# Kernel tuning notes

Hardware: AMD Instinct MI355X
Metric: run time of the kernel (lower is better)

The kernel has to match this reference:

```python
import jax, jax.numpy as jnp
import numpy as np


def _linear_init(key, fan_in, fan_out):
    k1, k2 = jax.random.split(key)
    sc = 1.0 / np.sqrt(fan_in)
    w = jax.random.uniform(k1, (fan_in, fan_out), jnp.float32, -sc, sc)
    b = jax.random.uniform(k2, (fan_out,), jnp.float32, -sc, sc)
    return w, b


def setup_inputs() -> dict:
    key = jax.random.key(0)
    ks = jax.random.split(key, 16)
    b, s, q, c, d = 8, 5, 15, 256, 4
    inp = {
        'support_xf': jax.random.normal(ks[0], (b, s, c, d, d), jnp.float32),
        'query_xf': jax.random.normal(ks[1], (b, q, c, d, d), jnp.float32),
        'support_y': jax.random.randint(ks[2], (b, s), 0, 5),
        'query_y': jax.random.randint(ks[3], (b, q), 0, 5),
    }
    g_dims = [(516, 256), (256, 256), (256, 256), (256, 256)]
    for i, (fi, fo) in enumerate(g_dims):
        w, bb = _linear_init(ks[4 + i], fi, fo)
        inp['g_w%d' % (i + 1)] = w
        inp['g_b%d' % (i + 1)] = bb
    f_dims = [(256, 256), (256, 256), (256, 29), (29, 1)]
    for i, (fi, fo) in enumerate(f_dims):
        w, bb = _linear_init(ks[8 + i], fi, fo)
        inp['f_w%d' % (i + 1)] = w
        inp['f_b%d' % (i + 1)] = bb
    return inp


def reference(support_xf, query_xf, support_y, query_y,
              g_w1, g_b1, g_w2, g_b2, g_w3, g_b3, g_w4, g_b4,
              f_w1, f_b1, f_w2, f_b2, f_w3, f_b3, f_w4, f_b4):
    b, s, c, d, _ = support_xf.shape
    q = query_xf.shape[1]
    d2 = d * d
    relu = jax.nn.relu
    # coord channels: ch0 = i/d (row), ch1 = j/d (col), shape [2, d, d]
    ii = jnp.arange(d, dtype=support_xf.dtype) / d
    coord = jnp.stack([jnp.broadcast_to(ii[:, None], (d, d)),
                       jnp.broadcast_to(ii[None, :], (d, d))], axis=0)
    sup = jnp.concatenate([support_xf, jnp.broadcast_to(coord, (b, s, 2, d, d))], axis=2)
    qry = jnp.concatenate([query_xf, jnp.broadcast_to(coord, (b, q, 2, d, d))], axis=2)
    cp = c + 2
    sup = sup.reshape(b, s, cp, d2).transpose(0, 1, 3, 2)  # [b,s,d2,cp]
    qry = qry.reshape(b, q, cp, d2).transpose(0, 1, 3, 2)  # [b,q,d2,cp]
    # pair[b,q,s,m,n] = concat(support feature at spatial n, query feature at spatial m)
    sup_e = jnp.broadcast_to(sup[:, None, :, None, :, :], (b, q, s, d2, d2, cp))
    qry_e = jnp.broadcast_to(qry[:, :, None, :, None, :], (b, q, s, d2, d2, cp))
    x = jnp.concatenate([sup_e, qry_e], axis=-1)  # [b,q,s,d2,d2,2*cp]
    # g MLP applied per pair
    x = relu(x @ g_w1 + g_b1)
    x = relu(x @ g_w2 + g_b2)
    x = relu(x @ g_w3 + g_b3)
    x = relu(x @ g_w4 + g_b4)
    xf = x.sum(axis=(3, 4))  # sum over d^4 pairs -> [b,q,s,256]
    # f MLP (Dropout is identity in eval mode)
    y = relu(xf @ f_w1 + f_b1)
    y = relu(y @ f_w2 + f_b2)
    y = relu(y @ f_w3 + f_b3)
    score = jax.nn.sigmoid(y @ f_w4 + f_b4)[..., 0]  # [b,q,s]
    label = (support_y[:, None, :] == query_y[:, :, None]).astype(score.dtype)
    loss = jnp.sum((label - score) ** 2) / b
    return loss
```

## Files before the change

### kernel.cpp

```cpp
#include <hip/hip_runtime.h>

typedef __attribute__((ext_vector_type(8))) __bf16 bf16x8;
typedef __attribute__((ext_vector_type(8))) short short8;
typedef __attribute__((ext_vector_type(4))) float f32x4;
typedef unsigned int u32;

static __device__ __forceinline__ unsigned short f2bf(float f) {
    u32 u = __float_as_uint(f);
    u += 0x7FFFu + ((u >> 16) & 1u);
    return (unsigned short)(u >> 16);
}
static __device__ __forceinline__ u32 cvt_pk_bf16(float lo, float hi) {
    u32 r;
    asm("v_cvt_pk_bf16_f32 %0, %1, %2" : "=v"(r) : "v"(lo), "v"(hi));
    return r;
}
static __device__ __forceinline__ bf16x8 as_bf16x8(short8 v) {
    return __builtin_bit_cast(bf16x8, v);
}
static __device__ __forceinline__ f32x4 mfma16(short8 a, short8 b, f32x4 c) {
    return __builtin_amdgcn_mfma_f32_16x16x32_bf16(as_bf16x8(a), as_bf16x8(b), c, 0, 0, 0);
}

#define NB 8
#define NS 5
#define NQ 15
#define A_OFF_F 0
#define B_OFF_F (640*256)
#define XF_OFF_F (B_OFF_F + 1920*256)
#define WF_OFF_BYTES ((XF_OFF_F + 600*1024)*4)
#define WF1_OFF_BYTES (WF_OFF_BYTES + 48*8192)
#define WFF_OFF_BYTES (WF1_OFF_BYTES + 32*9216)
#define WF3_OFF_BYTES (WFF_OFF_BYTES + 32*8192)

__global__ void kA(const float* __restrict__ w2, const float* __restrict__ w3,
                   const float* __restrict__ w4, const float* __restrict__ w1,
                   const float* __restrict__ fw1, const float* __restrict__ fw2,
                   const float* __restrict__ fw3,
                   unsigned short* __restrict__ wf, unsigned short* __restrict__ wf1,
                   unsigned short* __restrict__ wff, unsigned short* __restrict__ wf3) {
    int bid = blockIdx.x;
    int l = threadIdx.x;
    if (bid < 48) {
        int L = bid >> 4, tt = bid & 15;
        const float* W = (L == 0) ? w2 : ((L == 1) ? w3 : w4);
        int nn = tt * 16 + (l & 15);
        #pragma unroll
        for (int kk = 0; kk < 8; ++kk) {
            int k0 = kk * 32 + (l >> 4) * 8;
            short8 ov;
            #pragma unroll
            for (int j = 0; j < 8; ++j)
                ov[j] = (short)f2bf(W[(size_t)(k0 + j) * 256 + nn]);
            *(short8*)((char*)wf + (size_t)bid * 8192 + kk * 1024 + l * 16) = ov;
        }
        return;
    }
    if (bid < 80) {
        int c1 = bid - 48;
        int S = c1 >> 4, tt = c1 & 15;
        int nn = tt * 16 + (l & 15);
        for (int kk = 0; kk < 9; ++kk) {
            int k0 = kk * 32 + (l >> 4) * 8;
            short8 ov;
            #pragma unroll
            for (int j = 0; j < 8; ++j) {
                int kb = k0 + j;
                float v = (kb < 258) ? w1[(size_t)(S * 258 + kb) * 256 + nn] : 0.0f;
                ov[j] = (short)f2bf(v);
            }
            *(short8*)((char*)wf1 + (size_t)c1 * 9216 + kk * 1024 + l * 16) = ov;
        }
        return;
    }
    if (bid < 112) {
        int cid = bid - 80;
        int Lf = cid >> 4, tt = cid & 15;
        const float* W = (Lf == 0) ? fw1 : fw2;
        int nn = tt * 16 + (l & 15);
        #pragma unroll
        for (int kk = 0; kk < 8; ++kk) {
            int k0 = kk * 32 + (l >> 4) * 8;
            short8 ov;
            #pragma unroll
            for (int j = 0; j < 8; ++j)
                ov[j] = (short)f2bf(W[(size_t)(k0 + j) * 256 + nn]);
            *(short8*)((char*)wff + (size_t)cid * 8192 + kk * 1024 + l * 16) = ov;
        }
        return;
    }
    {
        int tt = bid - 112;
        int nn = tt * 16 + (l & 15);
        #pragma unroll
        for (int kk = 0; kk < 8; ++kk) {
            int k0 = kk * 32 + (l >> 4) * 8;
            short8 ov;
            #pragma unroll
            for (int j = 0; j < 8; ++j) {
                float v = (nn < 29) ? fw3[(size_t)(k0 + j) * 29 + nn] : 0.0f;
                ov[j] = (short)f2bf(v);
            }
            *(short8*)((char*)wf3 + (size_t)tt * 8192 + kk * 1024 + l * 16) = ov;
        }
    }
}

__launch_bounds__(512, 1)
__global__ void kB(const float* __restrict__ sup, const float* __restrict__ qry,
                   const unsigned short* __restrict__ wf1,
                   const float* __restrict__ gb1, float* __restrict__ ws) {
    __shared__ short Xf[18432];
    int bid = blockIdx.x;
    bool isA = (bid < 10);
    int S = isA ? 0 : 1;
    int cellbase = isA ? bid * 4 : (bid - 10) * 4;
    const float* src = isA ? sup : qry;
    float* dst0 = ws + (isA ? A_OFF_F : B_OFF_F);
    int t = threadIdx.x;
    int w = t >> 6, l = t & 63;
    int g = l >> 4, c = l & 15;
    char* Xb = (char*)Xf;
    const char* w1b = (const char*)wf1;

    for (int idx = w; idx < 36; idx += 8) {
        int m = idx / 9, kk = idx % 9;
        const float* xp = src + (size_t)(cellbase + m) * 4096;
        int kbase = kk * 32 + g * 8;
        float v[8];
        #pragma unroll
        for (int j = 0; j < 8; ++j) {
            int kb = kbase + j;
            float x;
            if (kb < 256)       x = xp[(size_t)kb * 16 + c];
            else if (kb == 256) x = (float)(c >> 2) * 0.25f;
            else if (kb == 257) x = (float)(c & 3) * 0.25f;
            else                x = 0.0f;
            v[j] = x;
        }
        uint4 hv;
        hv.x = cvt_pk_bf16(v[0], v[1]);
        hv.y = cvt_pk_bf16(v[2], v[3]);
        hv.z = cvt_pk_bf16(v[4], v[5]);
        hv.w = cvt_pk_bf16(v[6], v[7]);
        *(uint4*)(Xb + (size_t)(m * 9 + kk) * 1024 + l * 16) = hv;
    }
    __syncthreads();

    int wp = w >> 2, wn = w & 3;
    const char* wbase = w1b + (size_t)(S * 16 + wn * 4) * 9216;
    short8 wcur[4];
    #pragma unroll
    for (int tti = 0; tti < 4; ++tti)
        wcur[tti] = *(const short8*)(wbase + (size_t)tti * 9216 + l * 16);

    f32x4 acc[2][4];
    #pragma unroll
    for (int pg = 0; pg < 2; ++pg)
        #pragma unroll
        for (int tti = 0; tti < 4; ++tti)
            acc[pg][tti] = (f32x4){0.f, 0.f, 0.f, 0.f};

    #pragma unroll
    for (int kk = 0; kk < 9; ++kk) {
        int kn = kk + 1; if (kn > 8) kn = 8;
        short8 wnxt[4];
        #pragma unroll
        for (int tti = 0; tti < 4; ++tti)
            wnxt[tti] = *(const short8*)(wbase + (size_t)tti * 9216 + kn * 1024 + l * 16);
        #pragma unroll
        for (int pg = 0; pg < 2; ++pg) {
            short8 h = *(const short8*)(Xb + (size_t)((wp * 2 + pg) * 9 + kk) * 1024 + l * 16);
            #pragma unroll
            for (int tti = 0; tti < 4; ++tti)
                acc[pg][tti] = mfma16(wcur[tti], h, acc[pg][tti]);
        }
        #pragma unroll
        for (int tti = 0; tti < 4; ++tti) wcur[tti] = wnxt[tti];
    }

    #pragma unroll
    for (int tti = 0; tti < 4; ++tti) {
        int col0 = wn * 64 + tti * 16 + g * 4;
        float4 bv = {0.f, 0.f, 0.f, 0.f};
        if (S == 0) bv = *(const float4*)(gb1 + col0);
        #pragma unroll
        for (int pg = 0; pg < 2; ++pg) {
            int row = (cellbase + wp * 2 + pg) * 16 + c;
            float4 o;
            o.x = acc[pg][tti][0] + bv.x;
            o.y = acc[pg][tti][1] + bv.y;
            o.z = acc[pg][tti][2] + bv.z;
            o.w = acc[pg][tti][3] + bv.w;
            *(float4*)(dst0 + (size_t)row * 256 + col0) = o;
        }
    }
}

__launch_bounds__(512, 4)
__global__ void k3_g(const float* __restrict__ wsA, const float* __restrict__ wsB,
                     const unsigned short* __restrict__ wf,
                     const float* __restrict__ gb2, const float* __restrict__ gb3,
                     const float* __restrict__ gb4, float* __restrict__ xf) {
    __shared__ short Hf[32768];
    __shared__ float bs[768];
    int bid = blockIdx.x;
    int bqs = bid >> 1, half = bid & 1;
    int b = bqs / 75, rem = bqs % 75, qi = rem / 5, si = rem % 5;
    int t = threadIdx.x;
    int w = t >> 6, l = t & 63;
    int g = l >> 4, c = l & 15;
    int wp = w >> 2, wn = w & 3;
    char* Hb = (char*)Hf;
    const char* wfb = (const char*)wf;

    if (t < 256) { bs[t] = gb2[t]; bs[256 + t] = gb3[t]; bs[512 + t] = gb4[t]; }

    short8 wcur[4];
    #pragma unroll
    for (int tti = 0; tti < 4; ++tti)
        wcur[tti] = *(const short8*)(wfb + (size_t)(wn * 4 + tti) * 8192 + l * 16);

    {
        const float* Arow = wsA + (size_t)(b * NS + si) * 4096 + c * 256;
        const float* Brow = wsB + (size_t)(b * NQ + qi) * 4096 + (half * 8 + w) * 256;
        #pragma unroll
        for (int kk = 0; kk < 8; ++kk) {
            const float* ap = Arow + kk * 32 + g * 8;
            const float* bp = Brow + kk * 32 + g * 8;
            float4 a0 = *(const float4*)ap, a1 = *(const float4*)(ap + 4);
            float4 b0 = *(const float4*)bp, b1 = *(const float4*)(bp + 4);
            uint4 hv;
            hv.x = cvt_pk_bf16(fmaxf(a0.x + b0.x, 0.f), fmaxf(a0.y + b0.y, 0.f));
            hv.y = cvt_pk_bf16(fmaxf(a0.z + b0.z, 0.f), fmaxf(a0.w + b0.w, 0.f));
            hv.z = cvt_pk_bf16(fmaxf(a1.x + b1.x, 0.f), fmaxf(a1.y + b1.y, 0.f));
            hv.w = cvt_pk_bf16(fmaxf(a1.z + b1.z, 0.f), fmaxf(a1.w + b1.w, 0.f));
            *(uint4*)(Hb + (size_t)(w * 8 + kk) * 1024 + l * 16) = hv;
        }
    }
    __syncthreads();

    #pragma unroll 1
    for (int L = 0; L < 3; ++L) {
        f32x4 acc[4][4];
        #pragma unroll
        for (int pg = 0; pg < 4; ++pg)
            #pragma unroll
            for (int tti = 0; tti < 4; ++tti)
                acc[pg][tti] = (f32x4){0.f, 0.f, 0.f, 0.f};

        #pragma unroll
        for (int kk = 0; kk < 8; ++kk) {
            int s = L * 8 + kk + 1; if (s > 23) s = 23;
            int Ln = s >> 3, kn = s & 7;
            short8 wnxt[4];
            #pragma unroll
            for (int tti = 0; tti < 4; ++tti)
                wnxt[tti] = *(const short8*)(wfb +
                    (size_t)(Ln * 16 + wn * 4 + tti) * 8192 + kn * 1024 + l * 16);
            #pragma unroll
            for (int pg = 0; pg < 4; ++pg) {
                short8 h = *(const short8*)(Hb +
                    (size_t)((wp * 4 + pg) * 8 + kk) * 1024 + l * 16);
                #pragma unroll
                for (int tti = 0; tti < 4; ++tti)
                    acc[pg][tti] = mfma16(wcur[tti], h, acc[pg][tti]);
            }
            #pragma unroll
            for (int tti = 0; tti < 4; ++tti) wcur[tti] = wnxt[tti];
        }

        float4 bv[4];
        #pragma unroll
        for (int tti = 0; tti < 4; ++tti)
            bv[tti] = *(const float4*)(bs + L * 256 + wn * 64 + tti * 16 + g * 4);

        if (L < 2) {
            __syncthreads();
            #pragma unroll
            for (int pg = 0; pg < 4; ++pg) {
                int m = wp * 4 + pg;
                #pragma unroll
                for (int tti = 0; tti < 4; ++tti) {
                    uint2 q;
                    q.x = cvt_pk_bf16(fmaxf(acc[pg][tti][0] + bv[tti].x, 0.f),
                                      fmaxf(acc[pg][tti][1] + bv[tti].y, 0.f));
                    q.y = cvt_pk_bf16(fmaxf(acc[pg][tti][2] + bv[tti].z, 0.f),
                                      fmaxf(acc[pg][tti][3] + bv[tti].w, 0.f));
                    int kk2 = wn * 2 + (tti >> 1);
                    int dlane = ((tti & 1) * 2 + (g >> 1)) * 16 + c;
                    *(uint2*)(Hb + (size_t)(m * 8 + kk2) * 1024 + dlane * 16 + (g & 1) * 8) = q;
                }
            }
            __syncthreads();
        } else {
            #pragma unroll
            for (int tti = 0; tti < 4; ++tti) {
                float s0 = 0.f, s1 = 0.f, s2 = 0.f, s3 = 0.f;
                #pragma unroll
                for (int pg = 0; pg < 4; ++pg) {
                    s0 += fmaxf(acc[pg][tti][0] + bv[tti].x, 0.f);
                    s1 += fmaxf(acc[pg][tti][1] + bv[tti].y, 0.f);
                    s2 += fmaxf(acc[pg][tti][2] + bv[tti].z, 0.f);
                    s3 += fmaxf(acc[pg][tti][3] + bv[tti].w, 0.f);
                }
                #pragma unroll
                for (int d = 1; d < 16; d <<= 1) {
                    s0 += __shfl_xor(s0, d); s1 += __shfl_xor(s1, d);
                    s2 += __shfl_xor(s2, d); s3 += __shfl_xor(s3, d);
                }
                if (c == 0) {
                    float4 o = {s0, s1, s2, s3};
                    *(float4*)(xf + (((size_t)bqs * 2 + half) * 2 + wp) * 256 +
                               wn * 64 + tti * 16 + g * 4) = o;
                }
            }
        }
    }
}

__launch_bounds__(512, 1)
__global__ void k4_f(const float* __restrict__ xf,
                     const unsigned short* __restrict__ wff,
                     const unsigned short* __restrict__ wf3,
                     const float* __restrict__ fb1, const float* __restrict__ fb2,
                     const float* __restrict__ fb3,
                     const float* __restrict__ fw4, const float* __restrict__ fb4,
                     const int* __restrict__ sy, const int* __restrict__ qy,
                     float* __restrict__ out) {
    __shared__ short Hf[16384];
    __shared__ float bs[512];
    __shared__ float bs3[32];
    __shared__ float y3[64][32];
    int bid = blockIdx.x;
    int t = threadIdx.x;
    int w = t >> 6, l = t & 63;
    int g = l >> 4, c = l & 15;
    char* Hb = (char*)Hf;
    const char* wfb = (const char*)wff;

    bs[t & 511] = (t < 256) ? fb1[t] : fb2[t - 256];
    if (t < 32) bs3[t] = (t < 29) ? fb3[t] : 0.0f;

    for (int fi = w; fi < 32; fi += 8) {
        int m = fi >> 3, kk = fi & 7;
        int row = bid * 64 + m * 16 + c;
        if (row > 599) row = 599;
        const float* xr = xf + (size_t)row * 1024;
        int kb = kk * 32 + g * 8;
        float v[8];
        #pragma unroll
        for (int j = 0; j < 8; ++j) {
            int f = kb + j;
            v[j] = xr[f] + xr[256 + f] + xr[512 + f] + xr[768 + f];
        }
        uint4 hv;
        hv.x = cvt_pk_bf16(v[0], v[1]);
        hv.y = cvt_pk_bf16(v[2], v[3]);
        hv.z = cvt_pk_bf16(v[4], v[5]);
        hv.w = cvt_pk_bf16(v[6], v[7]);
        *(uint4*)(Hb + (size_t)(m * 8 + kk) * 1024 + l * 16) = hv;
    }
    __syncthreads();

    int wp = w >> 2, wn = w & 3;
    short8 wcur[4];
    #pragma unroll
    for (int tti = 0; tti < 4; ++tti)
        wcur[tti] = *(const short8*)(wfb + (size_t)(wn * 4 + tti) * 8192 + l * 16);

    #pragma unroll 1
    for (int L = 0; L < 2; ++L) {
        f32x4 acc[2][4];
        #pragma unroll
        for (int pg = 0; pg < 2; ++pg)
            #pragma unroll
            for (int tti = 0; tti < 4; ++tti)
                acc[pg][tti] = (f32x4){0.f, 0.f, 0.f, 0.f};

        #pragma unroll
        for (int kk = 0; kk < 8; ++kk) {
            int s = L * 8 + kk + 1; if (s > 15) s = 15;
            int Ln = s >> 3, kn = s & 7;
            short8 wnxt[4];
            #pragma unroll
            for (int tti = 0; tti < 4; ++tti)
                wnxt[tti] = *(const short8*)(wfb +
                    (size_t)(Ln * 16 + wn * 4 + tti) * 8192 + kn * 1024 + l * 16);
            #pragma unroll
            for (int pg = 0; pg < 2; ++pg) {
                short8 h = *(const short8*)(Hb +
                    (size_t)((wp * 2 + pg) * 8 + kk) * 1024 + l * 16);
                #pragma unroll
                for (int tti = 0; tti < 4; ++tti)
                    acc[pg][tti] = mfma16(wcur[tti], h, acc[pg][tti]);
            }
            #pragma unroll
            for (int tti = 0; tti < 4; ++tti) wcur[tti] = wnxt[tti];
        }

        float4 bv[4];
        #pragma unroll
        for (int tti = 0; tti < 4; ++tti)
            bv[tti] = *(const float4*)(bs + L * 256 + wn * 64 + tti * 16 + g * 4);

        __syncthreads();
        #pragma unroll
        for (int pg = 0; pg < 2; ++pg) {
            int m = wp * 2 + pg;
            #pragma unroll
            for (int tti = 0; tti < 4; ++tti) {
                uint2 q;
                q.x = cvt_pk_bf16(fmaxf(acc[pg][tti][0] + bv[tti].x, 0.f),
                                  fmaxf(acc[pg][tti][1] + bv[tti].y, 0.f));
                q.y = cvt_pk_bf16(fmaxf(acc[pg][tti][2] + bv[tti].z, 0.f),
                                  fmaxf(acc[pg][tti][3] + bv[tti].w, 0.f));
                int kk2 = wn * 2 + (tti >> 1);
                int dlane = ((tti & 1) * 2 + (g >> 1)) * 16 + c;
                *(uint2*)(Hb + (size_t)(m * 8 + kk2) * 1024 + dlane * 16 + (g & 1) * 8) = q;
            }
        }
        __syncthreads();
    }

    {
        int m = w >> 1, tt = w & 1;
        f32x4 a3 = {0.f, 0.f, 0.f, 0.f};
        #pragma unroll
        for (int kk = 0; kk < 8; ++kk) {
            short8 wv = *(const short8*)((const char*)wf3 +
                (size_t)(tt * 8 + kk) * 1024 + l * 16);
            short8 h = *(const short8*)(Hb + (size_t)(m * 8 + kk) * 1024 + l * 16);
            a3 = mfma16(wv, h, a3);
        }
        #pragma unroll
        for (int r = 0; r < 4; ++r) {
            int oc = tt * 16 + g * 4 + r;
            float v = a3[r] + bs3[oc];
            y3[m * 16 + c][oc] = v > 0.f ? v : 0.f;
        }
    }
    __syncthreads();

    if (t < 64) {
        int bqs = bid * 64 + t;
        if (bqs < 600) {
            float z = fb4[0];
            #pragma unroll
            for (int k = 0; k < 29; ++k) z += y3[t][k] * fw4[k];
            float score = 1.0f / (1.0f + __expf(-z));
            int b = bqs / 75, rem = bqs % 75, qi = rem / 5, si = rem % 5;
            float label = (sy[b * NS + si] == qy[b * NQ + qi]) ? 1.0f : 0.0f;
            float d = label - score;
            atomicAdd(out, d * d * 0.125f);
        }
    }
}

extern "C" void kernel_launch(void* const* d_in, const int* in_sizes, int n_in,
                              void* d_out, int out_size, void* d_ws, size_t ws_size,
                              hipStream_t stream) {
    const float* sup = (const float*)d_in[0];
    const float* qry = (const float*)d_in[1];
    const int*   sy  = (const int*)d_in[2];
    const int*   qy  = (const int*)d_in[3];
    const float* gw1 = (const float*)d_in[4];
    const float* gb1 = (const float*)d_in[5];
    const float* gw2 = (const float*)d_in[6];
    const float* gb2 = (const float*)d_in[7];
    const float* gw3 = (const float*)d_in[8];
    const float* gb3 = (const float*)d_in[9];
    const float* gw4 = (const float*)d_in[10];
    const float* gb4 = (const float*)d_in[11];
    const float* fw1 = (const float*)d_in[12];
    const float* fb1 = (const float*)d_in[13];
    const float* fw2 = (const float*)d_in[14];
    const float* fb2 = (const float*)d_in[15];
    const float* fw3 = (const float*)d_in[16];
    const float* fb3 = (const float*)d_in[17];
    const float* fw4 = (const float*)d_in[18];
    const float* fb4 = (const float*)d_in[19];

    float* ws = (float*)d_ws;
    float* A  = ws + A_OFF_F;
    float* B  = ws + B_OFF_F;
    float* xf = ws + XF_OFF_F;
    unsigned short* wf  = (unsigned short*)((char*)d_ws + WF_OFF_BYTES);
    unsigned short* wf1 = (unsigned short*)((char*)d_ws + WF1_OFF_BYTES);
    unsigned short* wff = (unsigned short*)((char*)d_ws + WFF_OFF_BYTES);
    unsigned short* wf3 = (unsigned short*)((char*)d_ws + WF3_OFF_BYTES);
    float* out = (float*)d_out;

    hipMemsetAsync(out, 0, sizeof(float), stream);

    kA<<<114, 64, 0, stream>>>(gw2, gw3, gw4, gw1, fw1, fw2, fw3, wf, wf1, wff, wf3);
    kB<<<40, 512, 0, stream>>>(sup, qry, wf1, gb1, ws);
    k3_g<<<1200, 512, 0, stream>>>(A, B, wf, gb2, gb3, gb4, xf);
    k4_f<<<10, 512, 0, stream>>>(xf, wff, wf3, fb1, fb2, fb3, fw4, fb4, sy, qy, out);
}
```

Baseline: 118.9 us.

## Split prep kernels: spread layer-1 GEMM over more blocks, fold weight packing and memset

```diff
diff --git a/kernel.cpp b/kernel.cpp
--- a/kernel.cpp
+++ b/kernel.cpp
@@ -33,106 +33,105 @@
 #define WFF_OFF_BYTES (WF1_OFF_BYTES + 32*9216)
 #define WF3_OFF_BYTES (WFF_OFF_BYTES + 32*8192)
 
-__global__ void kA(const float* __restrict__ w2, const float* __restrict__ w3,
-                   const float* __restrict__ w4, const float* __restrict__ w1,
+__global__ void kA(const float* __restrict__ w1, unsigned short* __restrict__ wf1) {
+    int c1 = blockIdx.x;
+    int l = threadIdx.x;
+    int S = c1 >> 4, tt = c1 & 15;
+    int nn = tt * 16 + (l & 15);
+    for (int kk = 0; kk < 9; ++kk) {
+        int k0 = kk * 32 + (l >> 4) * 8;
+        short8 ov;
+        #pragma unroll
+        for (int j = 0; j < 8; ++j) {
+            int kb = k0 + j;
+            float v = (kb < 258) ? w1[(size_t)(S * 258 + kb) * 256 + nn] : 0.0f;
+            ov[j] = (short)f2bf(v);
+        }
+        *(short8*)((char*)wf1 + (size_t)c1 * 9216 + kk * 1024 + l * 16) = ov;
+    }
+}
+
+__global__ void kB(const float* __restrict__ sup, const float* __restrict__ qry,
+                   const unsigned short* __restrict__ wf1, const float* __restrict__ gb1,
+                   const float* __restrict__ w2, const float* __restrict__ w3,
+                   const float* __restrict__ w4,
                    const float* __restrict__ fw1, const float* __restrict__ fw2,
                    const float* __restrict__ fw3,
-                   unsigned short* __restrict__ wf, unsigned short* __restrict__ wf1,
-                   unsigned short* __restrict__ wff, unsigned short* __restrict__ wf3) {
+                   float* __restrict__ ws, unsigned short* __restrict__ wf,
+                   unsigned short* __restrict__ wff, unsigned short* __restrict__ wf3,
+                   float* __restrict__ out) {
+    __shared__ short Xf[4608];
     int bid = blockIdx.x;
-    int l = threadIdx.x;
-    if (bid < 48) {
-        int L = bid >> 4, tt = bid & 15;
-        const float* W = (L == 0) ? w2 : ((L == 1) ? w3 : w4);
-        int nn = tt * 16 + (l & 15);
-        #pragma unroll
-        for (int kk = 0; kk < 8; ++kk) {
-            int k0 = kk * 32 + (l >> 4) * 8;
-            short8 ov;
-            #pragma unroll
-            for (int j = 0; j < 8; ++j)
-                ov[j] = (short)f2bf(W[(size_t)(k0 + j) * 256 + nn]);
-            *(short8*)((char*)wf + (size_t)bid * 8192 + kk * 1024 + l * 16) = ov;
-        }
-        return;
-    }
-    if (bid < 80) {
-        int c1 = bid - 48;
-        int S = c1 >> 4, tt = c1 & 15;
-        int nn = tt * 16 + (l & 15);
-        for (int kk = 0; kk < 9; ++kk) {
-            int k0 = kk * 32 + (l >> 4) * 8;
-            short8 ov;
-            #pragma unroll
-            for (int j = 0; j < 8; ++j) {
-                int kb = k0 + j;
-                float v = (kb < 258) ? w1[(size_t)(S * 258 + kb) * 256 + nn] : 0.0f;
-                ov[j] = (short)f2bf(v);
-            }
-            *(short8*)((char*)wf1 + (size_t)c1 * 9216 + kk * 1024 + l * 16) = ov;
-        }
-        return;
-    }
-    if (bid < 112) {
-        int cid = bid - 80;
-        int Lf = cid >> 4, tt = cid & 15;
-        const float* W = (Lf == 0) ? fw1 : fw2;
-        int nn = tt * 16 + (l & 15);
-        #pragma unroll
-        for (int kk = 0; kk < 8; ++kk) {
-            int k0 = kk * 32 + (l >> 4) * 8;
-            short8 ov;
-            #pragma unroll
-            for (int j = 0; j < 8; ++j)
-                ov[j] = (short)f2bf(W[(size_t)(k0 + j) * 256 + nn]);
-            *(short8*)((char*)wff + (size_t)cid * 8192 + kk * 1024 + l * 16) = ov;
-        }
-        return;
-    }
-    {
-        int tt = bid - 112;
-        int nn = tt * 16 + (l & 15);
-        #pragma unroll
-        for (int kk = 0; kk < 8; ++kk) {
-            int k0 = kk * 32 + (l >> 4) * 8;
-            short8 ov;
-            #pragma unroll
-            for (int j = 0; j < 8; ++j) {
-                float v = (nn < 29) ? fw3[(size_t)(k0 + j) * 29 + nn] : 0.0f;
-                ov[j] = (short)f2bf(v);
-            }
-            *(short8*)((char*)wf3 + (size_t)tt * 8192 + kk * 1024 + l * 16) = ov;
-        }
-    }
-}
-
-__launch_bounds__(512, 1)
-__global__ void kB(const float* __restrict__ sup, const float* __restrict__ qry,
-                   const unsigned short* __restrict__ wf1,
-                   const float* __restrict__ gb1, float* __restrict__ ws) {
-    __shared__ short Xf[18432];
-    int bid = blockIdx.x;
-    bool isA = (bid < 10);
-    int S = isA ? 0 : 1;
-    int cellbase = isA ? bid * 4 : (bid - 10) * 4;
-    const float* src = isA ? sup : qry;
-    float* dst0 = ws + (isA ? A_OFF_F : B_OFF_F);
     int t = threadIdx.x;
     int w = t >> 6, l = t & 63;
     int g = l >> 4, c = l & 15;
+
+    if (bid >= 160) {
+        if (bid < 172) {
+            int cid = (bid - 160) * 4 + w;
+            int L = cid >> 4, tt = cid & 15;
+            const float* W = (L == 0) ? w2 : ((L == 1) ? w3 : w4);
+            int nn = tt * 16 + (l & 15);
+            #pragma unroll
+            for (int kk = 0; kk < 8; ++kk) {
+                int k0 = kk * 32 + (l >> 4) * 8;
+                short8 ov;
+                #pragma unroll
+                for (int j = 0; j < 8; ++j)
+                    ov[j] = (short)f2bf(W[(size_t)(k0 + j) * 256 + nn]);
+                *(short8*)((char*)wf + (size_t)cid * 8192 + kk * 1024 + l * 16) = ov;
+            }
+        } else if (bid == 172) {
+            if (w < 2) {
+                int tt = w;
+                int nn = tt * 16 + (l & 15);
+                #pragma unroll
+                for (int kk = 0; kk < 8; ++kk) {
+                    int k0 = kk * 32 + (l >> 4) * 8;
+                    short8 ov;
+                    #pragma unroll
+                    for (int j = 0; j < 8; ++j) {
+                        float v = (nn < 29) ? fw3[(size_t)(k0 + j) * 29 + nn] : 0.0f;
+                        ov[j] = (short)f2bf(v);
+                    }
+                    *(short8*)((char*)wf3 + (size_t)tt * 8192 + kk * 1024 + l * 16) = ov;
+                }
+            } else if (w == 2 && l == 0) {
+                out[0] = 0.0f;
+            }
+        } else {
+            int cid = (bid - 173) * 4 + w;
+            int Lf = cid >> 4, tt = cid & 15;
+            const float* W = (Lf == 0) ? fw1 : fw2;
+            int nn = tt * 16 + (l & 15);
+            #pragma unroll
+            for (int kk = 0; kk < 8; ++kk) {
+                int k0 = kk * 32 + (l >> 4) * 8;
+                short8 ov;
+                #pragma unroll
+                for (int j = 0; j < 8; ++j)
+                    ov[j] = (short)f2bf(W[(size_t)(k0 + j) * 256 + nn]);
+                *(short8*)((char*)wff + (size_t)cid * 8192 + kk * 1024 + l * 16) = ov;
+            }
+        }
+        return;
+    }
+
+    bool isA = (bid < 40);
+    int S = isA ? 0 : 1;
+    int cell = isA ? bid : (bid - 40);
+    const float* src = (isA ? sup : qry) + (size_t)cell * 4096;
+    float* dst0 = ws + (isA ? A_OFF_F : B_OFF_F);
     char* Xb = (char*)Xf;
-    const char* w1b = (const char*)wf1;
-
-    for (int idx = w; idx < 36; idx += 8) {
-        int m = idx / 9, kk = idx % 9;
-        const float* xp = src + (size_t)(cellbase + m) * 4096;
+
+    for (int kk = w; kk < 9; kk += 4) {
         int kbase = kk * 32 + g * 8;
         float v[8];
         #pragma unroll
         for (int j = 0; j < 8; ++j) {
             int kb = kbase + j;
             float x;
-            if (kb < 256)       x = xp[(size_t)kb * 16 + c];
+            if (kb < 256)       x = src[(size_t)kb * 16 + c];
             else if (kb == 256) x = (float)(c >> 2) * 0.25f;
             else if (kb == 257) x = (float)(c & 3) * 0.25f;
             else                x = 0.0f;
@@ -143,23 +142,19 @@
         hv.y = cvt_pk_bf16(v[2], v[3]);
         hv.z = cvt_pk_bf16(v[4], v[5]);
         hv.w = cvt_pk_bf16(v[6], v[7]);
-        *(uint4*)(Xb + (size_t)(m * 9 + kk) * 1024 + l * 16) = hv;
+        *(uint4*)(Xb + (size_t)kk * 1024 + l * 16) = hv;
     }
     __syncthreads();
 
-    int wp = w >> 2, wn = w & 3;
-    const char* wbase = w1b + (size_t)(S * 16 + wn * 4) * 9216;
+    const char* wbase = (const char*)wf1 + (size_t)(S * 16 + w * 4) * 9216;
     short8 wcur[4];
     #pragma unroll
     for (int tti = 0; tti < 4; ++tti)
         wcur[tti] = *(const short8*)(wbase + (size_t)tti * 9216 + l * 16);
 
-    f32x4 acc[2][4];
-    #pragma unroll
-    for (int pg = 0; pg < 2; ++pg)
-        #pragma unroll
-        for (int tti = 0; tti < 4; ++tti)
-            acc[pg][tti] = (f32x4){0.f, 0.f, 0.f, 0.f};
+    f32x4 acc[4];
+    #pragma unroll
+    for (int tti = 0; tti < 4; ++tti) acc[tti] = (f32x4){0.f, 0.f, 0.f, 0.f};
 
     #pragma unroll
     for (int kk = 0; kk < 9; ++kk) {
@@ -168,32 +163,26 @@
         #pragma unroll
         for (int tti = 0; tti < 4; ++tti)
             wnxt[tti] = *(const short8*)(wbase + (size_t)tti * 9216 + kn * 1024 + l * 16);
-        #pragma unroll
-        for (int pg = 0; pg < 2; ++pg) {
-            short8 h = *(const short8*)(Xb + (size_t)((wp * 2 + pg) * 9 + kk) * 1024 + l * 16);
-            #pragma unroll
-            for (int tti = 0; tti < 4; ++tti)
-                acc[pg][tti] = mfma16(wcur[tti], h, acc[pg][tti]);
-        }
+        short8 h = *(const short8*)(Xb + (size_t)kk * 1024 + l * 16);
+        #pragma unroll
+        for (int tti = 0; tti < 4; ++tti)
+            acc[tti] = mfma16(wcur[tti], h, acc[tti]);
         #pragma unroll
         for (int tti = 0; tti < 4; ++tti) wcur[tti] = wnxt[tti];
     }
 
     #pragma unroll
     for (int tti = 0; tti < 4; ++tti) {
-        int col0 = wn * 64 + tti * 16 + g * 4;
+        int col0 = w * 64 + tti * 16 + g * 4;
         float4 bv = {0.f, 0.f, 0.f, 0.f};
         if (S == 0) bv = *(const float4*)(gb1 + col0);
-        #pragma unroll
-        for (int pg = 0; pg < 2; ++pg) {
-            int row = (cellbase + wp * 2 + pg) * 16 + c;
-            float4 o;
-            o.x = acc[pg][tti][0] + bv.x;
-            o.y = acc[pg][tti][1] + bv.y;
-            o.z = acc[pg][tti][2] + bv.z;
-            o.w = acc[pg][tti][3] + bv.w;
-            *(float4*)(dst0 + (size_t)row * 256 + col0) = o;
-        }
+        int row = cell * 16 + c;
+        float4 o;
+        o.x = acc[tti][0] + bv.x;
+        o.y = acc[tti][1] + bv.y;
+        o.z = acc[tti][2] + bv.z;
+        o.w = acc[tti][3] + bv.w;
+        *(float4*)(dst0 + (size_t)row * 256 + col0) = o;
     }
 }
 
@@ -491,10 +480,9 @@
     unsigned short* wf3 = (unsigned short*)((char*)d_ws + WF3_OFF_BYTES);
     float* out = (float*)d_out;
 
-    hipMemsetAsync(out, 0, sizeof(float), stream);
-
-    kA<<<114, 64, 0, stream>>>(gw2, gw3, gw4, gw1, fw1, fw2, fw3, wf, wf1, wff, wf3);
-    kB<<<40, 512, 0, stream>>>(sup, qry, wf1, gb1, ws);
+    kA<<<32, 64, 0, stream>>>(gw1, wf1);
+    kB<<<181, 256, 0, stream>>>(sup, qry, wf1, gb1, gw2, gw3, gw4,
+                                fw1, fw2, fw3, ws, wf, wff, wf3, out);
     k3_g<<<1200, 512, 0, stream>>>(A, B, wf, gb2, gb3, gb4, xf);
     k4_f<<<10, 512, 0, stream>>>(xf, wff, wf3, fb1, fb2, fb3, fw4, fb4, sy, qy, out);
 }
```

Result: faster. 111.7 us, median of 3 (-6.0%).
